# Kernel tuning notes

Hardware: AMD Instinct MI355X
Metric: run time of the kernel (lower is better)

Reference implementation:

```python
import jax, jax.numpy as jnp
import numpy as np

B, S, E, H = 2, 2048, 1024, 16
D = E // H  # head_dim = 64


def setup_inputs() -> dict:
    key = jax.random.key(0)
    ks = jax.random.split(key, 6)
    scale = 1.0 / np.sqrt(E)
    return {
        "x": jax.random.normal(ks[0], (B, S, E), dtype=jnp.float32),
        "Wqkv_w": jax.random.normal(ks[1], (3 * E, E), dtype=jnp.float32) * scale,
        "Wqkv_b": jax.random.normal(ks[2], (3 * E,), dtype=jnp.float32) * 0.01,
        "out_w": jax.random.normal(ks[3], (E, E), dtype=jnp.float32) * scale,
        "out_b": jax.random.normal(ks[4], (E,), dtype=jnp.float32) * 0.01,
        "distance_decay": jax.random.normal(ks[5], (1,), dtype=jnp.float32),
    }


def reference(x, Wqkv_w, Wqkv_b, out_w, out_b, distance_decay):
    b, s, e = x.shape
    # fused QKV projection: (b, s, 3e) -> three (b, h, s, d)
    qkv = x @ Wqkv_w.T + Wqkv_b
    qkv = qkv.reshape(b, s, 3, H, D).transpose(2, 0, 3, 1, 4)  # (3, b, h, s, d)
    q, k, v = qkv[0], qkv[1], qkv[2]
    # scores scaled by 1/sqrt(head_dim)
    scores = jnp.einsum("bhsd,bhtd->bhst", q, k) / jnp.sqrt(jnp.asarray(D, x.dtype))
    # multiplicative exponential distance decay: exp(-|a| * |i-j|)
    idx = jnp.arange(s, dtype=x.dtype)
    dist = jnp.abs(idx[:, None] - idx[None, :])  # (s, s)
    decay = jnp.exp(-jnp.abs(distance_decay[0]) * dist)
    scores = scores * decay  # broadcast over (b, h)
    attn = jax.nn.softmax(scores, axis=-1)
    out = jnp.einsum("bhst,bhtd->bhsd", attn, v)  # (b, h, s, d)
    out = out.transpose(0, 2, 1, 3).reshape(b, s, e)  # (b, s, e)
    return out @ out_w.T + out_b
```

## Files before the change

### kernel.cpp

```cpp
#include <hip/hip_runtime.h>
#include <hip/hip_bf16.h>

#define BN 2
#define SDIM 2048
#define EDIM 1024
#define HN 16
#define DDIM 64

typedef __attribute__((ext_vector_type(8))) short bfrag;
typedef __attribute__((ext_vector_type(4))) float ffrag;

__device__ __forceinline__ ffrag mfma16(bfrag a, bfrag b, ffrag c) {
    return __builtin_amdgcn_mfma_f32_16x16x32_bf16(a, b, c, 0, 0, 0);
}

__device__ __forceinline__ ushort f2bf(float f) {
    union { float f; unsigned u; } un;
    un.f = f;
    unsigned u = un.u;
    u += 0x7fffu + ((u >> 16) & 1u);
    return (ushort)(u >> 16);
}

__device__ __forceinline__ uint pkbf2(float a, float b) {
    __hip_bfloat162 h = __float22bfloat162_rn(make_float2(a, b));
    union { __hip_bfloat162 h; uint u; } cv;
    cv.h = h;
    return cv.u;
}

__device__ __forceinline__ void gld16(const void* g, void* l) {
    __builtin_amdgcn_global_load_lds((const __attribute__((address_space(1))) void*)g,
                                     (__attribute__((address_space(3))) void*)l,
                                     16, 0, 0);
}

__global__ __launch_bounds__(256) void to_bf16_3(const float* __restrict__ a, ushort* __restrict__ oa, int na,
                                                 const float* __restrict__ b, ushort* __restrict__ ob, int nb,
                                                 const float* __restrict__ c, ushort* __restrict__ oc, int nc) {
    int i = (blockIdx.x * 256 + threadIdx.x) * 4;
    const float* src;
    ushort* dst;
    if (i < na)                { src = a + i;            dst = oa + i; }
    else if (i < na + nb)      { src = b + (i - na);     dst = ob + (i - na); }
    else if (i < na + nb + nc) { src = c + (i - na - nb); dst = oc + (i - na - nb); }
    else return;
    float4 v = *(const float4*)src;
    uint2 u;
    u.x = pkbf2(v.x, v.y);
    u.y = pkbf2(v.z, v.w);
    *(uint2*)dst = u;
}

template <int MODE, int MI>
__global__ __launch_bounds__(256) void gemm_bt(const ushort* __restrict__ A,
                                               const ushort* __restrict__ Bt,
                                               const float* __restrict__ bias,
                                               void* __restrict__ Cout,
                                               int M, int N, int K) {
    __shared__ ushort As[MI * 32 * 64];
    __shared__ ushort Bs[128 * 64];

    const int tid  = threadIdx.x;
    const int wave = tid >> 6;
    const int lane = tid & 63;
    const int ln16 = lane & 15;
    const int quad = lane >> 4;
    const int wm = wave >> 1, wn = wave & 1;
    const int bm = blockIdx.x * (MI * 32);
    const int bn = blockIdx.y * 128;

    ffrag acc[MI][4];
#pragma unroll
    for (int mi = 0; mi < MI; ++mi)
#pragma unroll
        for (int ni = 0; ni < 4; ++ni)
            acc[mi][ni] = (ffrag){0.f, 0.f, 0.f, 0.f};

    for (int k0 = 0; k0 < K; k0 += 64) {
#pragma unroll
        for (int p = 0; p < MI; ++p) {
            int g0 = p * 256 + wave * 64;
            int g  = g0 + lane;
            int r  = g >> 3;
            int c  = ((g & 7) - r) & 7;
            gld16(A + (size_t)(bm + r) * K + k0 + c * 8, (ushort*)As + g0 * 8);
        }
#pragma unroll
        for (int p = 0; p < 4; ++p) {
            int g0 = p * 256 + wave * 64;
            int g  = g0 + lane;
            int r  = g >> 3;
            int c  = ((g & 7) - r) & 7;
            gld16(Bt + (size_t)(bn + r) * K + k0 + c * 8, (ushort*)Bs + g0 * 8);
        }
        __syncthreads();

#pragma unroll
        for (int kb = 0; kb < 2; ++kb) {
            bfrag af[MI], bf[4];
#pragma unroll
            for (int mi = 0; mi < MI; ++mi) {
                int r = wm * (MI * 16) + mi * 16 + ln16;
                af[mi] = *(const bfrag*)&As[r * 64 + ((kb * 4 + quad + r) & 7) * 8];
            }
#pragma unroll
            for (int ni = 0; ni < 4; ++ni) {
                int r = wn * 64 + ni * 16 + ln16;
                bf[ni] = *(const bfrag*)&Bs[r * 64 + ((kb * 4 + quad + r) & 7) * 8];
            }
#pragma unroll
            for (int mi = 0; mi < MI; ++mi)
#pragma unroll
                for (int ni = 0; ni < 4; ++ni)
                    acc[mi][ni] = mfma16(af[mi], bf[ni], acc[mi][ni]);
        }
        __syncthreads();
    }

#pragma unroll
    for (int mi = 0; mi < MI; ++mi) {
#pragma unroll
        for (int ni = 0; ni < 4; ++ni) {
            int col = bn + wn * 64 + ni * 16 + ln16;
            float bc = bias[col];
            int row0 = bm + wm * (MI * 16) + mi * 16 + quad * 4;
            if (MODE == 0) {
#pragma unroll
                for (int reg = 0; reg < 4; ++reg)
                    ((float*)Cout)[(size_t)(row0 + reg) * N + col] = acc[mi][ni][reg] + bc;
            } else {
                int which = col >> 10;
                int rem = col & 1023;
                int h = rem >> 6;
                int d = rem & 63;
                int b = row0 >> 11;
                int s0 = row0 & 2047;
                if (which == 2) {
                    float v0 = acc[mi][ni][0] + bc, v1 = acc[mi][ni][1] + bc;
                    float v2 = acc[mi][ni][2] + bc, v3 = acc[mi][ni][3] + bc;
                    uint2 pk;
                    pk.x = pkbf2(v0, v1);
                    pk.y = pkbf2(v2, v3);
                    size_t dst = 2ull * (BN * HN * SDIM * DDIM) +
                                 (((size_t)(b * HN + h)) * DDIM + d) * SDIM + s0;
                    *(uint2*)((ushort*)Cout + dst) = pk;
                } else {
                    float sc = (which == 0) ? 0.125f : 1.f;
#pragma unroll
                    for (int reg = 0; reg < 4; ++reg) {
                        float v = (acc[mi][ni][reg] + bc) * sc;
                        size_t dst = (size_t)which * (BN * HN * SDIM * DDIM) +
                                     (((size_t)(b * HN + h)) * SDIM + s0 + reg) * DDIM + d;
                        ((ushort*)Cout)[dst] = f2bf(v);
                    }
                }
            }
        }
    }
}

__global__ __launch_bounds__(256) void vsum_tiles(const ushort* __restrict__ Vtb,
                                                  float* __restrict__ T) {
    const int bh   = blockIdx.x;
    const int tile = blockIdx.y * 4 + (threadIdx.x >> 6);
    const int d    = threadIdx.x & 63;
    const ushort* row = Vtb + ((size_t)bh * DDIM + d) * SDIM + tile * 64;
    float s = 0.f;
#pragma unroll
    for (int j = 0; j < 64; j += 8) {
        uint4 v = *(const uint4*)(row + j);
        ushort tmp[8];
        *(uint4*)tmp = v;
#pragma unroll
        for (int e = 0; e < 8; ++e) {
            union { float f; uint u; } c;
            c.u = ((uint)tmp[e]) << 16;
            s += c.f;
        }
    }
    T[((size_t)bh * 32 + tile) * 64 + d] = s;
}

__global__ __launch_bounds__(512, 4) void flash_attn(const ushort* __restrict__ Qb,
                                                     const ushort* __restrict__ Kb,
                                                     const ushort* __restrict__ Vtb,
                                                     const float* __restrict__ decay_ptr,
                                                     const float* __restrict__ T,
                                                     ushort* __restrict__ Ob) {
    __shared__ ushort KVs[2][2][4096];
    __shared__ ushort Pb[128][72];
    __shared__ float  Fv[64];

    const int tid  = threadIdx.x;
    const int wave = tid >> 6;
    const int lane = tid & 63;
    const int ln16 = lane & 15;
    const int quad = lane >> 4;

    const int bh = blockIdx.y;
    const int q0 = blockIdx.x * 128;
    const size_t head_off = (size_t)bh * SDIM * DDIM;
    const float absa = fabsf(decay_ptr[0]);
    const float LOG2E = 1.442695041f;
    const float M0L2 = -17.3123404f;
    const float E12 = 6.144212353e-6f;

    int Dstar = (absa > 1e-5f) ? (int)ceilf(16.0f / absa) : (4 * SDIM);
    int lo = q0 - 63 - Dstar; if (lo < 0) lo = 0;
    int hi = q0 + 127 + Dstar; if (hi > SDIM - 1) hi = SDIM - 1;
    const int tlo = lo >> 6;
    const int thi = hi >> 6;
    const int ntiles = thi - tlo + 1;

    if (tid < 64) {
        const float* Tp = T + (size_t)bh * 32 * 64;
        float s = 0.f;
        for (int k = 0; k < tlo; ++k)      s += Tp[k * 64 + tid];
        for (int k = thi + 1; k < 32; ++k) s += Tp[k * 64 + tid];
        Fv[tid] = s;
    }

    auto stageKV = [&](int t0, int buf) {
        int g0 = wave * 64;
        int g  = g0 + lane;
        int r  = g >> 3;
        int c  = (g - r) & 7;
        gld16(Kb  + head_off + (size_t)(t0 + r) * DDIM + c * 8,
              (ushort*)&KVs[buf][0][0] + g0 * 8);
        gld16(Vtb + head_off + (size_t)r * SDIM + t0 + c * 8,
              (ushort*)&KVs[buf][1][0] + g0 * 8);
    };

#pragma unroll
    for (int p = 0; p < 2; ++p) {
        int idx = p * 512 + tid;
        int r = idx >> 3, c = (idx & 7) * 8;
        *(uint4*)&Pb[r][c] = *(const uint4*)(Qb + head_off + (size_t)(q0 + r) * DDIM + c);
    }
    stageKV(tlo * 64, 0);
    __syncthreads();

    bfrag aq[2];
#pragma unroll
    for (int kb = 0; kb < 2; ++kb)
        aq[kb] = *(const bfrag*)&Pb[wave * 16 + ln16][kb * 32 + quad * 8];

    bfrag ones;
#pragma unroll
    for (int i = 0; i < 8; ++i) ones[i] = (short)0x3F80;

    float EcB[4], FcB[4], Epw[4], Fpw[4];
#pragma unroll
    for (int reg = 0; reg < 4; ++reg) {
        int cr = quad * 4 + reg;
        EcB[reg] = __expf(-absa * (float)(15 - cr));
        FcB[reg] = __expf(-absa * (float)cr);
    }
#pragma unroll
    for (int ni = 0; ni < 4; ++ni) {
        Epw[ni] = __expf(-absa * (float)(16 * (3 - ni)));
        Fpw[ni] = __expf(-absa * (float)(16 * ni));
    }
    const float Er = __expf(-absa * (float)ln16);
    const float Fr = __expf(-absa * (float)(15 - ln16));

    ffrag lacc = (ffrag){0.f, 0.f, 0.f, 0.f};
    ffrag o[4];
#pragma unroll
    for (int ni = 0; ni < 4; ++ni) o[ni] = (ffrag){0.f, 0.f, 0.f, 0.f};

    const int m = wave * 16 + ln16;

    for (int it = 0; it < ntiles; ++it) {
        const int t0 = (tlo + it) * 64;
        const int buf = it & 1;
        if (it + 1 < ntiles) stageKV(t0 + 64, buf ^ 1);

        const ushort* Kt = &KVs[buf][0][0];
        const ushort* Vt = &KVs[buf][1][0];

        ffrag sc[4];
#pragma unroll
        for (int ni = 0; ni < 4; ++ni) {
            ffrag a = (ffrag){0.f, 0.f, 0.f, 0.f};
            const int rk = ni * 16 + ln16;
#pragma unroll
            for (int kb = 0; kb < 2; ++kb) {
                bfrag kf = *(const bfrag*)&Kt[rk * 64 + ((kb * 4 + quad + rk) & 7) * 8];
                a = mfma16(kf, aq[kb], a);
            }
            sc[ni] = a;
        }

        const int ds = q0 + wave * 16 - t0;
        float hh = 0.f;
        if (ds >= 64)       hh = __expf(-absa * (float)(ds - 63)) * Er * LOG2E;
        else if (ds <= -16) hh = __expf(-absa * (float)(-ds - 15)) * Fr * LOG2E;

#pragma unroll
        for (int ni = 0; ni < 4; ++ni) {
            float f0, f1, f2, f3;
            if (ds >= 64) {
                float hn = hh * Epw[ni];
                f0 = hn * EcB[0]; f1 = hn * EcB[1]; f2 = hn * EcB[2]; f3 = hn * EcB[3];
            } else if (ds <= -16) {
                float hn = hh * Fpw[ni];
                f0 = hn * FcB[0]; f1 = hn * FcB[1]; f2 = hn * FcB[2]; f3 = hn * FcB[3];
            } else {
                int c0 = ni * 16 + quad * 4;
                f0 = __expf(-absa * fabsf((float)(ds + ln16 - c0)))     * LOG2E;
                f1 = __expf(-absa * fabsf((float)(ds + ln16 - c0 - 1))) * LOG2E;
                f2 = __expf(-absa * fabsf((float)(ds + ln16 - c0 - 2))) * LOG2E;
                f3 = __expf(-absa * fabsf((float)(ds + ln16 - c0 - 3))) * LOG2E;
            }
            float p0 = exp2f(fmaf(sc[ni][0], f0, M0L2));
            float p1 = exp2f(fmaf(sc[ni][1], f1, M0L2));
            float p2 = exp2f(fmaf(sc[ni][2], f2, M0L2));
            float p3 = exp2f(fmaf(sc[ni][3], f3, M0L2));
            uint2 pk;
            pk.x = pkbf2(p0, p1);
            pk.y = pkbf2(p2, p3);
            *(uint2*)&Pb[m][ni * 16 + quad * 4] = pk;
        }

        bfrag ap[2];
#pragma unroll
        for (int kb = 0; kb < 2; ++kb)
            ap[kb] = *(const bfrag*)&Pb[m][kb * 32 + quad * 8];

#pragma unroll
        for (int kb = 0; kb < 2; ++kb)
            lacc = mfma16(ones, ap[kb], lacc);
#pragma unroll
        for (int ni = 0; ni < 4; ++ni) {
            const int rv = ni * 16 + ln16;
#pragma unroll
            for (int kb = 0; kb < 2; ++kb) {
                bfrag vf = *(const bfrag*)&Vt[rv * 64 + ((kb * 4 + quad + rv) & 7) * 8];
                o[ni] = mfma16(vf, ap[kb], o[ni]);
            }
        }
        __syncthreads();
    }

    const float farl = E12 * (float)(SDIM - 64 * ntiles);
    const float inv = 1.f / (lacc[0] + farl);
    const int b = bh / HN, h = bh % HN;
    const int s = q0 + m;
    ushort* dst = Ob + ((size_t)(b * SDIM + s)) * EDIM + h * DDIM + quad * 4;
#pragma unroll
    for (int ni = 0; ni < 4; ++ni) {
        int d0 = ni * 16 + quad * 4;
        float v0 = (o[ni][0] + E12 * Fv[d0 + 0]) * inv;
        float v1 = (o[ni][1] + E12 * Fv[d0 + 1]) * inv;
        float v2 = (o[ni][2] + E12 * Fv[d0 + 2]) * inv;
        float v3 = (o[ni][3] + E12 * Fv[d0 + 3]) * inv;
        uint2 pk;
        pk.x = pkbf2(v0, v1);
        pk.y = pkbf2(v2, v3);
        *(uint2*)(dst + ni * 16) = pk;
    }
}

extern "C" void kernel_launch(void* const* d_in, const int* in_sizes, int n_in,
                              void* d_out, int out_size, void* d_ws, size_t ws_size,
                              hipStream_t stream) {
    const float* x      = (const float*)d_in[0];
    const float* Wqkv_w = (const float*)d_in[1];
    const float* Wqkv_b = (const float*)d_in[2];
    const float* out_w  = (const float*)d_in[3];
    const float* out_b  = (const float*)d_in[4];
    const float* dd     = (const float*)d_in[5];

    char* ws = (char*)d_ws;
    const size_t MB = 1024 * 1024;
    ushort* xb    = (ushort*)(ws + 0 * MB);
    ushort* wqkvb = (ushort*)(ws + 8 * MB);
    ushort* owb   = (ushort*)(ws + 14 * MB);
    ushort* qkvb  = (ushort*)(ws + 16 * MB);
    ushort* ob    = (ushort*)(ws + 40 * MB);
    float*  Tp    = (float*)(ws + 0 * MB);

    const int n_x = BN * SDIM * EDIM;
    const int n_w = 3 * EDIM * EDIM;
    const int n_o = EDIM * EDIM;
    const int HSD = BN * HN * SDIM * DDIM;

    to_bf16_3<<<(n_x + n_w + n_o) / 1024, 256, 0, stream>>>(
        x, xb, n_x, Wqkv_w, wqkvb, n_w, out_w, owb, n_o);

    gemm_bt<1, 4><<<dim3(32, 24), 256, 0, stream>>>(xb, wqkvb, Wqkv_b, (void*)qkvb,
                                                    BN * SDIM, 3 * EDIM, EDIM);

    vsum_tiles<<<dim3(32, 8), 256, 0, stream>>>(qkvb + 2 * HSD, Tp);

    flash_attn<<<dim3(SDIM / 128, BN * HN), 512, 0, stream>>>(
        qkvb, qkvb + HSD, qkvb + 2 * HSD, dd, Tp, ob);

    gemm_bt<0, 2><<<dim3(64, 8), 256, 0, stream>>>(ob, owb, out_b, d_out,
                                                   BN * SDIM, EDIM, EDIM);
}
```

Measured before the change: 165.9 us.

## Replace QKV GEMM with 256x192-tile, 8-wave, software-pipelined kernel

Adds a dedicated QKV projection GEMM that uses 256x192 block tiles with 512 threads. It double-buffers LDS, staggers the global-to-LDS loads two k-steps ahead, interleaves them between MFMA phases, and raises wave priority during MFMA bursts. The aim is more data reuse per tile, with load latency hidden behind compute. In exchange it launches only 256 blocks and uses heavy register and LDS pressure, so occupancy is lower and hand-placed waitcnt counts must stay correct.

```diff
diff --git a/kernel.cpp b/kernel.cpp
--- a/kernel.cpp
+++ b/kernel.cpp
@@ -160,6 +160,150 @@
     }
 }
 
+template <int UNUSED>
+__global__ __launch_bounds__(512, 2) void gemm256_qkv(const ushort* __restrict__ A,
+                                                      const ushort* __restrict__ Bt,
+                                                      const float* __restrict__ bias,
+                                                      ushort* __restrict__ Cout,
+                                                      int M, int N, int K) {
+    constexpr int BM = 256, BNT = 192;
+    constexpr int A_USH = BM * 64;
+    constexpr int B_USH = BNT * 64;
+    constexpr int BUF_USH = A_USH + B_USH;
+    __shared__ ushort lds[2 * BUF_USH];
+
+    const int tid  = threadIdx.x;
+    const int wave = tid >> 6;
+    const int lane = tid & 63;
+    const int ln16 = lane & 15;
+    const int quad = lane >> 4;
+    const int wm   = wave >> 2;
+    const int wn   = wave & 3;
+    const int bm   = blockIdx.x * BM;
+    const int bn   = blockIdx.y * BNT;
+
+    const int r0 = tid >> 3;
+    const int c0 = ((tid & 7) - r0) & 7;
+    const ushort* Abase = A  + (size_t)(bm + r0) * K + c0 * 8;
+    const ushort* Bbase = Bt + (size_t)(bn + r0) * K + c0 * 8;
+    const int ldst0 = wave * 512;
+
+    const int Ra = wm * 128 + ln16;
+    const int Rb = wn * 48 + ln16;
+    int aoff[2], boff[2];
+#pragma unroll
+    for (int kb = 0; kb < 2; ++kb) {
+        aoff[kb] = Ra * 64 + ((kb * 4 + quad + Ra) & 7) * 8;
+        boff[kb] = A_USH + Rb * 64 + ((kb * 4 + quad + Rb) & 7) * 8;
+    }
+
+    ffrag acc[8][3];
+#pragma unroll
+    for (int mi = 0; mi < 8; ++mi)
+#pragma unroll
+        for (int ni = 0; ni < 3; ++ni)
+            acc[mi][ni] = (ffrag){0.f, 0.f, 0.f, 0.f};
+
+    const int nt = K >> 6;
+
+    auto stA = [&](int buf, int t, int rnd) {
+        gld16(Abase + (size_t)rnd * 64 * K + t * 64,
+              &lds[buf * BUF_USH + rnd * 4096 + ldst0]);
+    };
+    auto stB = [&](int buf, int t, int rnd) {
+        gld16(Bbase + (size_t)rnd * 64 * K + t * 64,
+              &lds[buf * BUF_USH + A_USH + rnd * 4096 + ldst0]);
+    };
+
+    stA(0, 0, 0); stA(0, 0, 1); stA(0, 0, 2); stA(0, 0, 3);
+    stB(0, 0, 0); stB(0, 0, 1); stB(0, 0, 2);
+    stA(1, 1, 0); stA(1, 1, 2);
+    stB(1, 1, 0); stB(1, 1, 1); stB(1, 1, 2);
+    asm volatile("s_waitcnt vmcnt(5)" ::: "memory");
+    __builtin_amdgcn_s_barrier();
+
+    for (int t = 0; t < nt; ++t) {
+        const int buf = t & 1;
+        const ushort* Al = &lds[buf * BUF_USH];
+        const bool h1 = (t + 1) < nt;
+        const bool h2 = (t + 2) < nt;
+        bfrag bfr[3][2];
+#pragma unroll
+        for (int p = 0; p < 4; ++p) {
+            bfrag afr[2][2];
+#pragma unroll
+            for (int m2 = 0; m2 < 2; ++m2)
+#pragma unroll
+                for (int kb = 0; kb < 2; ++kb)
+                    afr[m2][kb] = *(const bfrag*)(Al + aoff[kb] + (p * 2 + m2) * 1024);
+            if (p == 0) {
+#pragma unroll
+                for (int ni = 0; ni < 3; ++ni)
+#pragma unroll
+                    for (int kb = 0; kb < 2; ++kb)
+                        bfr[ni][kb] = *(const bfrag*)(Al + boff[kb] + ni * 1024);
+            }
+            if (p == 0 && h1) stA(buf ^ 1, t + 1, 1);
+            if (p == 1 && h1) stA(buf ^ 1, t + 1, 3);
+            if (p == 2 && h2) { stA(buf, t + 2, 0); stA(buf, t + 2, 2); stB(buf, t + 2, 0); }
+            if (p == 3 && h2) { stB(buf, t + 2, 1); stB(buf, t + 2, 2); }
+
+            __builtin_amdgcn_s_barrier();
+            asm volatile("s_waitcnt lgkmcnt(0)" ::: "memory");
+            __builtin_amdgcn_sched_barrier(0);
+            __builtin_amdgcn_s_setprio(1);
+#pragma unroll
+            for (int m2 = 0; m2 < 2; ++m2)
+#pragma unroll
+                for (int ni = 0; ni < 3; ++ni)
+#pragma unroll
+                    for (int kb = 0; kb < 2; ++kb)
+                        acc[p * 2 + m2][ni] = mfma16(afr[m2][kb], bfr[ni][kb], acc[p * 2 + m2][ni]);
+            __builtin_amdgcn_s_setprio(0);
+            if (p == 3) {
+                if (h2)      { asm volatile("s_waitcnt vmcnt(5)" ::: "memory"); }
+                else if (h1) { asm volatile("s_waitcnt vmcnt(0)" ::: "memory"); }
+            }
+            __builtin_amdgcn_s_barrier();
+        }
+    }
+
+#pragma unroll
+    for (int mi = 0; mi < 8; ++mi) {
+#pragma unroll
+        for (int ni = 0; ni < 3; ++ni) {
+            int col = bn + wn * 48 + ni * 16 + ln16;
+            float bc = bias[col];
+            int row0 = bm + wm * 128 + mi * 16 + quad * 4;
+            int which = col >> 10;
+            int rem = col & 1023;
+            int h = rem >> 6;
+            int d = rem & 63;
+            int b = row0 >> 11;
+            int s0 = row0 & 2047;
+            if (which == 2) {
+                float v0 = acc[mi][ni][0] + bc, v1 = acc[mi][ni][1] + bc;
+                float v2 = acc[mi][ni][2] + bc, v3 = acc[mi][ni][3] + bc;
+                uint2 pk;
+                pk.x = pkbf2(v0, v1);
+                pk.y = pkbf2(v2, v3);
+                size_t dst = 2ull * (BN * HN * SDIM * DDIM) +
+                             (((size_t)(b * HN + h)) * DDIM + d) * SDIM + s0;
+                *(uint2*)(Cout + dst) = pk;
+            } else {
+                float sc = (which == 0) ? 0.125f : 1.f;
+#pragma unroll
+                for (int reg = 0; reg < 4; ++reg) {
+                    float v = (acc[mi][ni][reg] + bc) * sc;
+                    size_t dst = (size_t)which * (BN * HN * SDIM * DDIM) +
+                                 (((size_t)(b * HN + h)) * SDIM + s0 + reg) * DDIM + d;
+                    Cout[dst] = f2bf(v);
+                }
+            }
+        }
+    }
+}
+
 __global__ __launch_bounds__(256) void vsum_tiles(const ushort* __restrict__ Vtb,
                                                   float* __restrict__ T) {
     const int bh   = blockIdx.x;
@@ -390,8 +534,8 @@
     to_bf16_3<<<(n_x + n_w + n_o) / 1024, 256, 0, stream>>>(
         x, xb, n_x, Wqkv_w, wqkvb, n_w, out_w, owb, n_o);
 
-    gemm_bt<1, 4><<<dim3(32, 24), 256, 0, stream>>>(xb, wqkvb, Wqkv_b, (void*)qkvb,
-                                                    BN * SDIM, 3 * EDIM, EDIM);
+    gemm256_qkv<0><<<dim3(16, 16), 512, 0, stream>>>(xb, wqkvb, Wqkv_b, qkvb,
+                                                     BN * SDIM, 3 * EDIM, EDIM);
 
     vsum_tiles<<<dim3(32, 8), 256, 0, stream>>>(qkvb + 2 * HSD, Tp);
 
```

New measurement: 166.7 us. Within noise of the previous version (+0.5%).
